# Performance work log

Measured on AMD Instinct MI355X. Metric: run time of the kernel, lower is better.

Reference implementation:

```python
import jax, jax.numpy as jnp
import numpy as np

CH = 256            # channels
IN_C = CH // 2      # 128
INTER_C = CH // 16  # 16
NUM_POINTS = 32
BN_EPS = 1e-5


def conv1x1(x, W, b=None):
    # x: [B,C,H,W], W: [O,C]
    y = jnp.einsum('oc,bchw->bohw', W, x)
    if b is not None:
        y = y + b[None, :, None, None]
    return y


def bilinear_sample(feat, sx, sy):
    """feat [B,C,H,W]; sx,sy [B,N,P] continuous index coords; border padding."""
    B, C, H, W = feat.shape
    x0f = jnp.floor(sx)
    y0f = jnp.floor(sy)
    wx = sx - x0f
    wy = sy - y0f
    x0 = jnp.clip(x0f.astype(jnp.int32), 0, W - 1)
    x1 = jnp.clip(x0f.astype(jnp.int32) + 1, 0, W - 1)
    y0 = jnp.clip(y0f.astype(jnp.int32), 0, H - 1)
    y1 = jnp.clip(y0f.astype(jnp.int32) + 1, 0, H - 1)
    feat_f = feat.reshape(B, C, H * W).transpose(0, 2, 1)  # [B,HW,C]

    def gather(yi, xi):
        idx = (yi * W + xi).reshape(B, -1)  # [B,N*P]
        return jnp.take_along_axis(feat_f, idx[:, :, None], axis=1)  # [B,N*P,C]

    wxf = wx.reshape(B, -1, 1)
    wyf = wy.reshape(B, -1, 1)
    out = (gather(y0, x0) * (1 - wxf) * (1 - wyf)
           + gather(y0, x1) * wxf * (1 - wyf)
           + gather(y1, x0) * (1 - wxf) * wyf
           + gather(y1, x1) * wxf * wyf)
    N, P = sx.shape[1], sx.shape[2]
    return out.reshape(B, N, P, C)


def multi_scale_attention(qf, vf, Wq, bq, Wk, bk, Wv, bv, Woff, boff):
    # deformable-style point-sampling attention with NUM_POINTS samples per query
    B, _, H, W = qf.shape
    N = H * W
    q = conv1x1(qf, Wq, bq).reshape(B, INTER_C, N).transpose(0, 2, 1)  # [B,N,Ci]
    k = conv1x1(vf, Wk, bk)                                            # [B,Ci,H,W]
    v = conv1x1(vf, Wv, bv)                                            # [B,Cv,H,W]
    off = conv1x1(qf, Woff, boff).reshape(B, NUM_POINTS, 2, N)
    off = off.transpose(0, 3, 1, 2)                                    # [B,N,P,2] (dx,dy)
    ys, xs = jnp.meshgrid(jnp.arange(H, dtype=qf.dtype),
                          jnp.arange(W, dtype=qf.dtype), indexing='ij')
    sx = xs.reshape(-1)[None, :, None] + off[..., 0]                   # [B,N,P]
    sy = ys.reshape(-1)[None, :, None] + off[..., 1]
    k_s = bilinear_sample(k, sx, sy)                                   # [B,N,P,Ci]
    v_s = bilinear_sample(v, sx, sy)                                   # [B,N,P,Cv]
    logits = jnp.einsum('bnc,bnpc->bnp', q, k_s) / jnp.sqrt(jnp.asarray(INTER_C, qf.dtype))
    attn = jax.nn.softmax(logits, axis=-1)
    out = jnp.einsum('bnp,bnpc->bnc', attn, v_s)                       # [B,N,Cv]
    return out.transpose(0, 2, 1).reshape(B, -1, H, W)


def setup_inputs() -> dict:
    key = jax.random.key(0)
    ks = jax.random.split(key, 12)
    B, Hl, Wl, Hh, Wh = 2, 64, 64, 32, 32
    s = 0.02
    return {
        'low_feature': jax.random.normal(ks[0], (B, CH, Hl, Wl), jnp.float32),
        'high_feature': jax.random.normal(ks[1], (B, CH, Hh, Wh), jnp.float32),
        'W1': jax.random.normal(ks[2], (IN_C, 2 * CH), jnp.float32) * s,
        'b1': jnp.zeros((IN_C,), jnp.float32),
        'W2': jax.random.normal(ks[3], (IN_C, CH), jnp.float32) * s,
        'b2': jnp.zeros((IN_C,), jnp.float32),
        'Wq': jax.random.normal(ks[4], (INTER_C, IN_C), jnp.float32) * s,
        'bq': jnp.zeros((INTER_C,), jnp.float32),
        'Wk': jax.random.normal(ks[5], (INTER_C, IN_C), jnp.float32) * s,
        'bk': jnp.zeros((INTER_C,), jnp.float32),
        'Wv': jax.random.normal(ks[6], (IN_C, IN_C), jnp.float32) * s,
        'bv': jnp.zeros((IN_C,), jnp.float32),
        'Woff': jax.random.normal(ks[7], (2 * NUM_POINTS, IN_C), jnp.float32) * 0.5,
        'boff': jnp.zeros((2 * NUM_POINTS,), jnp.float32),
        'Wb': jax.random.normal(ks[8], (CH, IN_C + CH), jnp.float32) * s,
        'gamma': jnp.ones((CH,), jnp.float32),
        'beta': jnp.zeros((CH,), jnp.float32),
        'rmean': jnp.zeros((CH,), jnp.float32),
        'rvar': jnp.ones((CH,), jnp.float32),
    }


def reference(low_feature, high_feature, W1, b1, W2, b2, Wq, bq, Wk, bk,
              Wv, bv, Woff, boff, Wb, gamma, beta, rmean, rvar):
    B, _, Hl, Wl = low_feature.shape
    # F.interpolate(mode='bilinear', align_corners=False) == jax.image half-pixel bilinear
    high_up = jax.image.resize(high_feature, (B, CH, Hl, Wl), method='bilinear')
    query_feature = conv1x1(jnp.concatenate([high_up, low_feature], axis=1), W1, b1)
    value_feature = conv1x1(high_up, W2, b2)
    value_feature = multi_scale_attention(query_feature, value_feature,
                                          Wq, bq, Wk, bk, Wv, bv, Woff, boff)
    x = conv1x1(jnp.concatenate([value_feature, high_up], axis=1), Wb)
    # BatchNorm (eval form) + ReLU
    x = (x - rmean[None, :, None, None]) * jax.lax.rsqrt(rvar + BN_EPS)[None, :, None, None]
    x = x * gamma[None, :, None, None] + beta[None, :, None, None]
    return jax.nn.relu(x)
```

## Files before the change

### kernel.cpp

```cpp
#include <hip/hip_runtime.h>
#include <hip/hip_bf16.h>

#define NL 4096
#define HH 32
#define WH 32

typedef __attribute__((ext_vector_type(8))) short s8v;
typedef __attribute__((ext_vector_type(4))) short s4v;
typedef __attribute__((ext_vector_type(4))) float f32x4;

static __device__ inline unsigned short f2bf(float x) {
  __hip_bfloat16 h = __float2bfloat16(x);
  return *reinterpret_cast<unsigned short*>(&h);
}
static __device__ inline float bfbits2f(unsigned int lo16) {
  unsigned int u = lo16 << 16;
  return *reinterpret_cast<float*>(&u);
}

__global__ __launch_bounds__(256) void convert_weights_k(
    const float* __restrict__ w1, const float* __restrict__ w2,
    const float* __restrict__ wq, const float* __restrict__ woff,
    const float* __restrict__ wk, const float* __restrict__ wv,
    const float* __restrict__ wb, short* __restrict__ dst) {
  int i = blockIdx.x * 256 + threadIdx.x;
  const float* src; int off;
  if      (i <  65536) { src = w1;   off = 0; }
  else if (i <  98304) { src = w2;   off = 65536; }
  else if (i < 100352) { src = wq;   off = 98304; }
  else if (i < 108544) { src = woff; off = 100352; }
  else if (i < 110592) { src = wk;   off = 108544; }
  else if (i < 126976) { src = wv;   off = 110592; }
  else if (i < 225280) { src = wb;   off = 126976; }
  else return;
  dst[i] = (short)f2bf(src[i - off]);
}

__global__ __launch_bounds__(256) void k1_fused(
    const float* __restrict__ low, const float* __restrict__ high,
    const short* __restrict__ wc,
    const float* __restrict__ b1, const float* __restrict__ b2,
    const float* __restrict__ bq, const float* __restrict__ boff,
    const float* __restrict__ bk, const float* __restrict__ bv,
    short* __restrict__ xh, float* __restrict__ q_t, float* __restrict__ k_t,
    float* __restrict__ off_t, short* __restrict__ v_t) {
  __shared__ short xin_s[16 * 520];
  __shared__ short qf_s[16 * 136];
  __shared__ short vf_s[16 * 136];
  const int tid = threadIdx.x;
  const int pix0 = blockIdx.x * 16;
  const int b = pix0 >> 12;
  const int n0 = pix0 & (NL - 1);

  {
    const int nl = tid & 15, cg = tid >> 4;
    const int n = n0 + nl;
    const int y = n >> 6, x = n & 63;
    float sx = x * 0.5f - 0.25f;
    float sy = y * 0.5f - 0.25f;
    float x0f = floorf(sx), y0f = floorf(sy);
    float wx = sx - x0f, wy = sy - y0f;
    int x0i = (int)x0f, y0i = (int)y0f;
    int x0c = min(WH - 1, max(0, x0i)), x1c = min(WH - 1, max(0, x0i + 1));
    int y0c = min(HH - 1, max(0, y0i)), y1c = min(HH - 1, max(0, y0i + 1));
    float w00 = (1.f - wy) * (1.f - wx), w01 = (1.f - wy) * wx;
    float w10 = wy * (1.f - wx),         w11 = wy * wx;
#pragma unroll
    for (int i = 0; i < 16; i++) {
      int c = cg * 16 + i;
      const float* f = high + (size_t)(b * 256 + c) * (HH * WH);
      float v = w00 * f[y0c * WH + x0c] + w01 * f[y0c * WH + x1c]
              + w10 * f[y1c * WH + x0c] + w11 * f[y1c * WH + x1c];
      xin_s[nl * 520 + c] = (short)f2bf(v);
      xin_s[nl * 520 + 256 + c] =
          (short)f2bf(low[(size_t)(b * 256 + c) * NL + n]);
    }
  }
  __syncthreads();

  {
    const int r = tid >> 4, c0 = (tid & 15) * 16;
    s8v v0 = *(const s8v*)(xin_s + r * 520 + c0);
    s8v v1 = *(const s8v*)(xin_s + r * 520 + c0 + 8);
    *(s8v*)(xh + (size_t)(pix0 + r) * 256 + c0) = v0;
    *(s8v*)(xh + (size_t)(pix0 + r) * 256 + c0 + 8) = v1;
  }

  const int wave = tid >> 6, lane = tid & 63;
  const int quad = lane >> 4, id = lane & 15;

  {
    f32x4 acc0 = (f32x4){0.f, 0.f, 0.f, 0.f};
    f32x4 acc1 = (f32x4){0.f, 0.f, 0.f, 0.f};
    const short* a0 = wc + (size_t)(wave * 32 + id) * 512 + quad * 8;
    const short* a1 = a0 + 16 * 512;
    const short* bp = xin_s + id * 520 + quad * 8;
#pragma unroll
    for (int kk = 0; kk < 512; kk += 32) {
      s8v bf = *(const s8v*)(bp + kk);
      acc0 = __builtin_amdgcn_mfma_f32_16x16x32_bf16(*(const s8v*)(a0 + kk), bf, acc0, 0, 0, 0);
      acc1 = __builtin_amdgcn_mfma_f32_16x16x32_bf16(*(const s8v*)(a1 + kk), bf, acc1, 0, 0, 0);
    }
    int m0 = wave * 32 + quad * 4;
    s4v o0, o1;
#pragma unroll
    for (int r = 0; r < 4; r++) {
      o0[r] = (short)f2bf(acc0[r] + b1[m0 + r]);
      o1[r] = (short)f2bf(acc1[r] + b1[m0 + 16 + r]);
    }
    *(s4v*)(qf_s + id * 136 + m0) = o0;
    *(s4v*)(qf_s + id * 136 + m0 + 16) = o1;
  }

  {
    f32x4 acc0 = (f32x4){0.f, 0.f, 0.f, 0.f};
    f32x4 acc1 = (f32x4){0.f, 0.f, 0.f, 0.f};
    const short* a0 = wc + 65536 + (size_t)(wave * 32 + id) * 256 + quad * 8;
    const short* a1 = a0 + 16 * 256;
    const short* bp = xin_s + id * 520 + quad * 8;
#pragma unroll
    for (int kk = 0; kk < 256; kk += 32) {
      s8v bf = *(const s8v*)(bp + kk);
      acc0 = __builtin_amdgcn_mfma_f32_16x16x32_bf16(*(const s8v*)(a0 + kk), bf, acc0, 0, 0, 0);
      acc1 = __builtin_amdgcn_mfma_f32_16x16x32_bf16(*(const s8v*)(a1 + kk), bf, acc1, 0, 0, 0);
    }
    int m0 = wave * 32 + quad * 4;
    s4v o0, o1;
#pragma unroll
    for (int r = 0; r < 4; r++) {
      o0[r] = (short)f2bf(acc0[r] + b2[m0 + r]);
      o1[r] = (short)f2bf(acc1[r] + b2[m0 + 16 + r]);
    }
    *(s4v*)(vf_s + id * 136 + m0) = o0;
    *(s4v*)(vf_s + id * 136 + m0 + 16) = o1;
  }
  __syncthreads();

  for (int f = wave; f < 14; f += 4) {
    const short* ap = wc + 98304 + (size_t)(f * 16 + id) * 128 + quad * 8;
    const short* bp = (f < 5 ? qf_s : vf_s) + id * 136 + quad * 8;
    f32x4 acc = (f32x4){0.f, 0.f, 0.f, 0.f};
#pragma unroll
    for (int kk = 0; kk < 128; kk += 32)
      acc = __builtin_amdgcn_mfma_f32_16x16x32_bf16(
          *(const s8v*)(ap + kk), *(const s8v*)(bp + kk), acc, 0, 0, 0);
    const int pix = pix0 + id;
    const int mq = quad * 4;
    if (f == 0) {
      f32x4 v;
#pragma unroll
      for (int r = 0; r < 4; r++) v[r] = acc[r] + bq[mq + r];
      *(f32x4*)(q_t + (size_t)pix * 16 + mq) = v;
    } else if (f < 5) {
      int m = (f - 1) * 16 + mq;
      f32x4 v;
#pragma unroll
      for (int r = 0; r < 4; r++) v[r] = acc[r] + boff[m + r];
      *(f32x4*)(off_t + (size_t)pix * 64 + m) = v;
    } else if (f == 5) {
      f32x4 v;
#pragma unroll
      for (int r = 0; r < 4; r++) v[r] = acc[r] + bk[mq + r];
      *(f32x4*)(k_t + (size_t)pix * 16 + mq) = v;
    } else {
      int m = (f - 6) * 16 + mq;
      s4v o;
#pragma unroll
      for (int r = 0; r < 4; r++) o[r] = (short)f2bf(acc[r] + bv[m + r]);
      *(s4v*)(v_t + (size_t)pix * 128 + m) = o;
    }
  }
}

template <int M, int K1, int K2, int MF>
__global__ __launch_bounds__(256) void finalg_k(
    const short* __restrict__ W,
    const short* __restrict__ B1, int sB1,
    const short* __restrict__ B2, int sB2,
    float* __restrict__ Y,
    const float* __restrict__ gamma, const float* __restrict__ beta,
    const float* __restrict__ rmean, const float* __restrict__ rvar) {
  constexpr int K = K1 + K2;
  const int tid = threadIdx.x;
  const int wave = tid >> 6, lane = tid & 63;
  const int quad = lane >> 4, id = lane & 15;
  const int n = blockIdx.x * 64 + wave * 16 + id;
  const int m0 = blockIdx.y * (MF * 16);

  f32x4 acc[MF];
#pragma unroll
  for (int mf = 0; mf < MF; mf++) acc[mf] = (f32x4){0.f, 0.f, 0.f, 0.f};

  const short* ap[MF];
#pragma unroll
  for (int mf = 0; mf < MF; mf++)
    ap[mf] = W + (size_t)(m0 + mf * 16 + id) * K + quad * 8;
  const short* bp = B1 + (size_t)n * sB1 + quad * 8;
#pragma unroll
  for (int kk = 0; kk < K1; kk += 32) {
    s8v bf = *(const s8v*)(bp + kk);
#pragma unroll
    for (int mf = 0; mf < MF; mf++)
      acc[mf] = __builtin_amdgcn_mfma_f32_16x16x32_bf16(
          *(const s8v*)(ap[mf] + kk), bf, acc[mf], 0, 0, 0);
  }
  const short* bp2 = B2 + (size_t)n * sB2 + quad * 8;
#pragma unroll
  for (int kk = 0; kk < K2; kk += 32) {
    s8v bf = *(const s8v*)(bp2 + kk);
#pragma unroll
    for (int mf = 0; mf < MF; mf++)
      acc[mf] = __builtin_amdgcn_mfma_f32_16x16x32_bf16(
          *(const s8v*)(ap[mf] + K1 + kk), bf, acc[mf], 0, 0, 0);
  }

  const int bb = n >> 12, nlow = n & (NL - 1);
#pragma unroll
  for (int mf = 0; mf < MF; mf++) {
    int mbase = m0 + mf * 16 + quad * 4;
#pragma unroll
    for (int r = 0; r < 4; r++) {
      int o = mbase + r;
      float s  = gamma[o] * rsqrtf(rvar[o] + 1e-5f);
      float sh = beta[o] - rmean[o] * s;
      Y[((size_t)bb * M + o) * NL + nlow] = fmaxf(fmaf(acc[mf][r], s, sh), 0.f);
    }
  }
}

__global__ __launch_bounds__(256) void attn_k(
    const float* __restrict__ q_t, const float* __restrict__ k_t,
    const short* __restrict__ v_t, const float* __restrict__ off_t,
    short* __restrict__ out) {
  const int lane = threadIdx.x;
  const int wav  = threadIdx.y;
  const int qidx = blockIdx.x * 4 + wav;
  const int b = qidx >> 12;
  const int n = qidx & (NL - 1);
  const int qy = n >> 6, qx = n & 63;

  __shared__ float s_w[4][32][4];
  __shared__ int   s_i[4][32][4];

  const float* qp = q_t + (size_t)qidx * 16;
  float qreg[16];
#pragma unroll
  for (int i = 0; i < 16; i += 4) {
    float4 t = *(const float4*)(qp + i);
    qreg[i] = t.x; qreg[i + 1] = t.y; qreg[i + 2] = t.z; qreg[i + 3] = t.w;
  }

  const int pt = lane >> 1;
  const int h = lane & 1;
  float2 dxy = *(const float2*)(off_t + (size_t)qidx * 64 + 2 * pt);
  float sx = (float)qx + dxy.x;
  float sy = (float)qy + dxy.y;
  float x0f = floorf(sx), y0f = floorf(sy);
  float wx = sx - x0f, wy = sy - y0f;
  int x0i = (int)x0f, y0i = (int)y0f;
  int x0 = min(63, max(0, x0i)), x1 = min(63, max(0, x0i + 1));
  int y0 = min(63, max(0, y0i)), y1 = min(63, max(0, y0i + 1));

  int   yr  = h ? y1 : y0;
  float wyr = h ? wy : (1.f - wy);
  int   pa = yr * 64 + x0, pb = yr * 64 + x1;
  float wa = wyr * (1.f - wx), wb = wyr * wx;

  const float* kb = k_t + (size_t)b * NL * 16;
  float da = 0.f, db = 0.f;
  {
    const float* ka = kb + (size_t)pa * 16;
    const float* kc = kb + (size_t)pb * 16;
#pragma unroll
    for (int i = 0; i < 16; i += 4) {
      float4 a4 = *(const float4*)(ka + i);
      float4 c4 = *(const float4*)(kc + i);
      da = fmaf(qreg[i], a4.x, da); da = fmaf(qreg[i + 1], a4.y, da);
      da = fmaf(qreg[i + 2], a4.z, da); da = fmaf(qreg[i + 3], a4.w, da);
      db = fmaf(qreg[i], c4.x, db); db = fmaf(qreg[i + 1], c4.y, db);
      db = fmaf(qreg[i + 2], c4.z, db); db = fmaf(qreg[i + 3], c4.w, db);
    }
  }
  float part = wa * da + wb * db;
  part += __shfl_xor(part, 1, 64);
  float logit = part * 0.25f;

  float m = logit;
#pragma unroll
  for (int s = 32; s > 0; s >>= 1) m = fmaxf(m, __shfl_xor(m, s, 64));
  float e = __expf(logit - m);
  float ssum = e;
#pragma unroll
  for (int s = 32; s > 0; s >>= 1) ssum += __shfl_xor(ssum, s, 64);
  float a = e * 2.f / ssum;

  s_w[wav][pt][2 * h + 0] = a * wa;
  s_w[wav][pt][2 * h + 1] = a * wb;
  s_i[wav][pt][2 * h + 0] = pa;
  s_i[wav][pt][2 * h + 1] = pb;

  const short* vb = v_t + (size_t)b * NL * 128;
  const int c = 2 * lane;
  float o0 = 0.f, o1 = 0.f;
  for (int pp = 0; pp < 32; pp++) {
#pragma unroll
    for (int t = 0; t < 4; t++) {
      float w  = s_w[wav][pp][t];
      int  pix = s_i[wav][pp][t];
      unsigned int u = *(const unsigned int*)(vb + (size_t)pix * 128 + c);
      o0 = fmaf(w, bfbits2f(u & 0xffffu), o0);
      o1 = fmaf(w, bfbits2f(u >> 16), o1);
    }
  }
  unsigned int pk = (unsigned int)f2bf(o0) | ((unsigned int)f2bf(o1) << 16);
  *(unsigned int*)(out + (size_t)qidx * 128 + c) = pk;
}

extern "C" void kernel_launch(void* const* d_in, const int* in_sizes, int n_in,
                              void* d_out, int out_size, void* d_ws, size_t ws_size,
                              hipStream_t stream) {
  const float* low   = (const float*)d_in[0];
  const float* high  = (const float*)d_in[1];
  const float* W1    = (const float*)d_in[2];
  const float* b1    = (const float*)d_in[3];
  const float* W2    = (const float*)d_in[4];
  const float* b2    = (const float*)d_in[5];
  const float* Wq    = (const float*)d_in[6];
  const float* bq    = (const float*)d_in[7];
  const float* Wk    = (const float*)d_in[8];
  const float* bk    = (const float*)d_in[9];
  const float* Wv    = (const float*)d_in[10];
  const float* bv    = (const float*)d_in[11];
  const float* Woff  = (const float*)d_in[12];
  const float* boff  = (const float*)d_in[13];
  const float* Wb    = (const float*)d_in[14];
  const float* gamma = (const float*)d_in[15];
  const float* beta  = (const float*)d_in[16];
  const float* rmean = (const float*)d_in[17];
  const float* rvar  = (const float*)d_in[18];
  float* out = (float*)d_out;

  short* ws    = (short*)d_ws;
  short* xh    = ws;
  short* v_t   = xh + 2097152;
  short* attn_t= v_t + 1048576;
  short* wc    = attn_t + 1048576;
  float* q_t   = (float*)(wc + 225280);
  float* k_t   = q_t + 131072;
  float* off_t = k_t + 131072;

  convert_weights_k<<<880, 256, 0, stream>>>(W1, W2, Wq, Woff, Wk, Wv, Wb, wc);
  k1_fused<<<512, 256, 0, stream>>>(low, high, wc, b1, b2, bq, boff, bk, bv,
                                    xh, q_t, k_t, off_t, v_t);
  attn_k<<<2048, dim3(64, 4), 0, stream>>>(q_t, k_t, v_t, off_t, attn_t);
  finalg_k<256, 128, 256, 2><<<dim3(128, 8), 256, 0, stream>>>(
      wc + 126976, attn_t, 128, xh, 256, out, gamma, beta, rmean, rvar);
}
```

Baseline: 160.7 us.

## Fuse deformable attention sampling with final projection GEMM and BN-ReLU

After: 160.4 us. About the same (-0.2%).

```diff
diff --git a/kernel.cpp b/kernel.cpp
--- a/kernel.cpp
+++ b/kernel.cpp
@@ -172,148 +172,140 @@
   }
 }
 
-template <int M, int K1, int K2, int MF>
-__global__ __launch_bounds__(256) void finalg_k(
-    const short* __restrict__ W,
-    const short* __restrict__ B1, int sB1,
-    const short* __restrict__ B2, int sB2,
-    float* __restrict__ Y,
+__global__ __launch_bounds__(256) void k2_fused(
+    const float* __restrict__ q_t, const float* __restrict__ k_t,
+    const short* __restrict__ v_t, const float* __restrict__ off_t,
+    const short* __restrict__ xh, const short* __restrict__ wb,
     const float* __restrict__ gamma, const float* __restrict__ beta,
-    const float* __restrict__ rmean, const float* __restrict__ rvar) {
-  constexpr int K = K1 + K2;
+    const float* __restrict__ rmean, const float* __restrict__ rvar,
+    float* __restrict__ out) {
+  __shared__ float s_w[4][32][4];
+  __shared__ int   s_i[4][32][4];
+  __shared__ short attn_s[16 * 136];
   const int tid = threadIdx.x;
   const int wave = tid >> 6, lane = tid & 63;
+  const int pix0 = blockIdx.x * 16;
+
+  const int pt = lane >> 1, h = lane & 1;
+  const int c = 2 * lane;
+  for (int jj = 0; jj < 4; jj++) {
+    const int qidx = pix0 + wave * 4 + jj;
+    const int b = qidx >> 12;
+    const int n = qidx & (NL - 1);
+    const int qy = n >> 6, qx = n & 63;
+
+    const float* qp = q_t + (size_t)qidx * 16;
+    float qreg[16];
+#pragma unroll
+    for (int i = 0; i < 16; i += 4) {
+      float4 t = *(const float4*)(qp + i);
+      qreg[i] = t.x; qreg[i + 1] = t.y; qreg[i + 2] = t.z; qreg[i + 3] = t.w;
+    }
+
+    float2 dxy = *(const float2*)(off_t + (size_t)qidx * 64 + 2 * pt);
+    float sx = (float)qx + dxy.x;
+    float sy = (float)qy + dxy.y;
+    float x0f = floorf(sx), y0f = floorf(sy);
+    float wx = sx - x0f, wy = sy - y0f;
+    int x0i = (int)x0f, y0i = (int)y0f;
+    int x0 = min(63, max(0, x0i)), x1 = min(63, max(0, x0i + 1));
+    int y0 = min(63, max(0, y0i)), y1 = min(63, max(0, y0i + 1));
+
+    int   yr  = h ? y1 : y0;
+    float wyr = h ? wy : (1.f - wy);
+    int   pa = yr * 64 + x0, pb = yr * 64 + x1;
+    float wa = wyr * (1.f - wx), wb_ = wyr * wx;
+
+    const float* kb = k_t + (size_t)b * NL * 16;
+    float da = 0.f, db = 0.f;
+    {
+      const float* ka = kb + (size_t)pa * 16;
+      const float* kc = kb + (size_t)pb * 16;
+#pragma unroll
+      for (int i = 0; i < 16; i += 4) {
+        float4 a4 = *(const float4*)(ka + i);
+        float4 c4 = *(const float4*)(kc + i);
+        da = fmaf(qreg[i], a4.x, da); da = fmaf(qreg[i + 1], a4.y, da);
+        da = fmaf(qreg[i + 2], a4.z, da); da = fmaf(qreg[i + 3], a4.w, da);
+        db = fmaf(qreg[i], c4.x, db); db = fmaf(qreg[i + 1], c4.y, db);
+        db = fmaf(qreg[i + 2], c4.z, db); db = fmaf(qreg[i + 3], c4.w, db);
+      }
+    }
+    float part = wa * da + wb_ * db;
+    part += __shfl_xor(part, 1, 64);
+    float logit = part * 0.25f;
+
+    float m = logit;
+#pragma unroll
+    for (int s = 32; s > 0; s >>= 1) m = fmaxf(m, __shfl_xor(m, s, 64));
+    float e = __expf(logit - m);
+    float ssum = e;
+#pragma unroll
+    for (int s = 32; s > 0; s >>= 1) ssum += __shfl_xor(ssum, s, 64);
+    float a = e * 2.f / ssum;
+
+    s_w[wave][pt][2 * h + 0] = a * wa;
+    s_w[wave][pt][2 * h + 1] = a * wb_;
+    s_i[wave][pt][2 * h + 0] = pa;
+    s_i[wave][pt][2 * h + 1] = pb;
+
+    const short* vb = v_t + (size_t)b * NL * 128;
+    float o0 = 0.f, o1 = 0.f;
+    for (int pp = 0; pp < 32; pp++) {
+#pragma unroll
+      for (int t = 0; t < 4; t++) {
+        float w  = s_w[wave][pp][t];
+        int  pix = s_i[wave][pp][t];
+        unsigned int u = *(const unsigned int*)(vb + (size_t)pix * 128 + c);
+        o0 = fmaf(w, bfbits2f(u & 0xffffu), o0);
+        o1 = fmaf(w, bfbits2f(u >> 16), o1);
+      }
+    }
+    unsigned int pk = (unsigned int)f2bf(o0) | ((unsigned int)f2bf(o1) << 16);
+    *(unsigned int*)(attn_s + (wave * 4 + jj) * 136 + c) = pk;
+  }
+  __syncthreads();
+
   const int quad = lane >> 4, id = lane & 15;
-  const int n = blockIdx.x * 64 + wave * 16 + id;
-  const int m0 = blockIdx.y * (MF * 16);
-
-  f32x4 acc[MF];
-#pragma unroll
-  for (int mf = 0; mf < MF; mf++) acc[mf] = (f32x4){0.f, 0.f, 0.f, 0.f};
-
-  const short* ap[MF];
-#pragma unroll
-  for (int mf = 0; mf < MF; mf++)
-    ap[mf] = W + (size_t)(m0 + mf * 16 + id) * K + quad * 8;
-  const short* bp = B1 + (size_t)n * sB1 + quad * 8;
-#pragma unroll
-  for (int kk = 0; kk < K1; kk += 32) {
-    s8v bf = *(const s8v*)(bp + kk);
-#pragma unroll
-    for (int mf = 0; mf < MF; mf++)
+  const int m0 = wave * 64;
+  const int pix = pix0 + id;
+
+  s8v bfr[12];
+#pragma unroll
+  for (int k4 = 0; k4 < 4; k4++)
+    bfr[k4] = *(const s8v*)(attn_s + id * 136 + quad * 8 + k4 * 32);
+#pragma unroll
+  for (int k8 = 0; k8 < 8; k8++)
+    bfr[4 + k8] = *(const s8v*)(xh + (size_t)pix * 256 + quad * 8 + k8 * 32);
+
+  f32x4 acc[4];
+#pragma unroll
+  for (int mf = 0; mf < 4; mf++) acc[mf] = (f32x4){0.f, 0.f, 0.f, 0.f};
+  const short* ap[4];
+#pragma unroll
+  for (int mf = 0; mf < 4; mf++)
+    ap[mf] = wb + (size_t)(m0 + mf * 16 + id) * 384 + quad * 8;
+
+#pragma unroll
+  for (int k = 0; k < 12; k++) {
+#pragma unroll
+    for (int mf = 0; mf < 4; mf++)
       acc[mf] = __builtin_amdgcn_mfma_f32_16x16x32_bf16(
-          *(const s8v*)(ap[mf] + kk), bf, acc[mf], 0, 0, 0);
-  }
-  const short* bp2 = B2 + (size_t)n * sB2 + quad * 8;
-#pragma unroll
-  for (int kk = 0; kk < K2; kk += 32) {
-    s8v bf = *(const s8v*)(bp2 + kk);
-#pragma unroll
-    for (int mf = 0; mf < MF; mf++)
-      acc[mf] = __builtin_amdgcn_mfma_f32_16x16x32_bf16(
-          *(const s8v*)(ap[mf] + K1 + kk), bf, acc[mf], 0, 0, 0);
-  }
-
-  const int bb = n >> 12, nlow = n & (NL - 1);
-#pragma unroll
-  for (int mf = 0; mf < MF; mf++) {
+          *(const s8v*)(ap[mf] + k * 32), bfr[k], acc[mf], 0, 0, 0);
+  }
+
+  const int bb = pix >> 12, nlow = pix & (NL - 1);
+#pragma unroll
+  for (int mf = 0; mf < 4; mf++) {
     int mbase = m0 + mf * 16 + quad * 4;
 #pragma unroll
     for (int r = 0; r < 4; r++) {
       int o = mbase + r;
       float s  = gamma[o] * rsqrtf(rvar[o] + 1e-5f);
       float sh = beta[o] - rmean[o] * s;
-      Y[((size_t)bb * M + o) * NL + nlow] = fmaxf(fmaf(acc[mf][r], s, sh), 0.f);
-    }
-  }
-}
-
-__global__ __launch_bounds__(256) void attn_k(
-    const float* __restrict__ q_t, const float* __restrict__ k_t,
-    const short* __restrict__ v_t, const float* __restrict__ off_t,
-    short* __restrict__ out) {
-  const int lane = threadIdx.x;
-  const int wav  = threadIdx.y;
-  const int qidx = blockIdx.x * 4 + wav;
-  const int b = qidx >> 12;
-  const int n = qidx & (NL - 1);
-  const int qy = n >> 6, qx = n & 63;
-
-  __shared__ float s_w[4][32][4];
-  __shared__ int   s_i[4][32][4];
-
-  const float* qp = q_t + (size_t)qidx * 16;
-  float qreg[16];
-#pragma unroll
-  for (int i = 0; i < 16; i += 4) {
-    float4 t = *(const float4*)(qp + i);
-    qreg[i] = t.x; qreg[i + 1] = t.y; qreg[i + 2] = t.z; qreg[i + 3] = t.w;
-  }
-
-  const int pt = lane >> 1;
-  const int h = lane & 1;
-  float2 dxy = *(const float2*)(off_t + (size_t)qidx * 64 + 2 * pt);
-  float sx = (float)qx + dxy.x;
-  float sy = (float)qy + dxy.y;
-  float x0f = floorf(sx), y0f = floorf(sy);
-  float wx = sx - x0f, wy = sy - y0f;
-  int x0i = (int)x0f, y0i = (int)y0f;
-  int x0 = min(63, max(0, x0i)), x1 = min(63, max(0, x0i + 1));
-  int y0 = min(63, max(0, y0i)), y1 = min(63, max(0, y0i + 1));
-
-  int   yr  = h ? y1 : y0;
-  float wyr = h ? wy : (1.f - wy);
-  int   pa = yr * 64 + x0, pb = yr * 64 + x1;
-  float wa = wyr * (1.f - wx), wb = wyr * wx;
-
-  const float* kb = k_t + (size_t)b * NL * 16;
-  float da = 0.f, db = 0.f;
-  {
-    const float* ka = kb + (size_t)pa * 16;
-    const float* kc = kb + (size_t)pb * 16;
-#pragma unroll
-    for (int i = 0; i < 16; i += 4) {
-      float4 a4 = *(const float4*)(ka + i);
-      float4 c4 = *(const float4*)(kc + i);
-      da = fmaf(qreg[i], a4.x, da); da = fmaf(qreg[i + 1], a4.y, da);
-      da = fmaf(qreg[i + 2], a4.z, da); da = fmaf(qreg[i + 3], a4.w, da);
-      db = fmaf(qreg[i], c4.x, db); db = fmaf(qreg[i + 1], c4.y, db);
-      db = fmaf(qreg[i + 2], c4.z, db); db = fmaf(qreg[i + 3], c4.w, db);
-    }
-  }
-  float part = wa * da + wb * db;
-  part += __shfl_xor(part, 1, 64);
-  float logit = part * 0.25f;
-
-  float m = logit;
-#pragma unroll
-  for (int s = 32; s > 0; s >>= 1) m = fmaxf(m, __shfl_xor(m, s, 64));
-  float e = __expf(logit - m);
-  float ssum = e;
-#pragma unroll
-  for (int s = 32; s > 0; s >>= 1) ssum += __shfl_xor(ssum, s, 64);
-  float a = e * 2.f / ssum;
-
-  s_w[wav][pt][2 * h + 0] = a * wa;
-  s_w[wav][pt][2 * h + 1] = a * wb;
-  s_i[wav][pt][2 * h + 0] = pa;
-  s_i[wav][pt][2 * h + 1] = pb;
-
-  const short* vb = v_t + (size_t)b * NL * 128;
-  const int c = 2 * lane;
-  float o0 = 0.f, o1 = 0.f;
-  for (int pp = 0; pp < 32; pp++) {
-#pragma unroll
-    for (int t = 0; t < 4; t++) {
-      float w  = s_w[wav][pp][t];
-      int  pix = s_i[wav][pp][t];
-      unsigned int u = *(const unsigned int*)(vb + (size_t)pix * 128 + c);
-      o0 = fmaf(w, bfbits2f(u & 0xffffu), o0);
-      o1 = fmaf(w, bfbits2f(u >> 16), o1);
-    }
-  }
-  unsigned int pk = (unsigned int)f2bf(o0) | ((unsigned int)f2bf(o1) << 16);
-  *(unsigned int*)(out + (size_t)qidx * 128 + c) = pk;
+      out[((size_t)bb * 256 + o) * NL + nlow] = fmaxf(fmaf(acc[mf][r], s, sh), 0.f);
+    }
+  }
 }
 
 extern "C" void kernel_launch(void* const* d_in, const int* in_sizes, int n_in,
@@ -343,8 +335,7 @@
   short* ws    = (short*)d_ws;
   short* xh    = ws;
   short* v_t   = xh + 2097152;
-  short* attn_t= v_t + 1048576;
-  short* wc    = attn_t + 1048576;
+  short* wc    = v_t + 1048576;
   float* q_t   = (float*)(wc + 225280);
   float* k_t   = q_t + 131072;
   float* off_t = k_t + 131072;
@@ -352,7 +343,6 @@
   convert_weights_k<<<880, 256, 0, stream>>>(W1, W2, Wq, Woff, Wk, Wv, Wb, wc);
   k1_fused<<<512, 256, 0, stream>>>(low, high, wc, b1, b2, bq, boff, bk, bv,
                                     xh, q_t, k_t, off_t, v_t);
-  attn_k<<<2048, dim3(64, 4), 0, stream>>>(q_t, k_t, v_t, off_t, attn_t);
-  finalg_k<256, 128, 256, 2><<<dim3(128, 8), 256, 0, stream>>>(
-      wc + 126976, attn_t, 128, xh, 256, out, gamma, beta, rmean, rvar);
-}
+  k2_fused<<<512, 256, 0, stream>>>(q_t, k_t, v_t, off_t, xh, wc + 126976,
+                                    gamma, beta, rmean, rvar, out);
+}
```
